# Performance work log

Measured on AMD Instinct MI355X. Metric: run time of the kernel, lower is better.

The kernel has to match this reference:

```python
import jax, jax.numpy as jnp
import numpy as np
import math

Re = 0.15
DX = 1.0
UB = -1.0
NZ, NY, NX = 64, 256, 256
DT = 0.5
ITERATION = 2

def conv3(x, w, stride=1):
    return jax.lax.conv_general_dilated(x, w, (stride, stride, stride), 'VALID', dimension_numbers=('NCDHW', 'OIDHW', 'NCDHW'))

def pad1(x):
    return jnp.pad(x, ((0, 0), (0, 0), (1, 1), (1, 1), (1, 1)))

def bc_u(u):
    p = pad1(u)
    p = p.at[0, 0, :, :, 0].set(UB)
    p = p.at[0, 0, :, :, -1].set(UB)
    p = p.at[0, 0, :, 0, :].set(p[0, 0, :, 1, :])
    p = p.at[0, 0, :, -1, :].set(p[0, 0, :, -2, :])
    p = p.at[0, 0, 0, :, :].set(0.0)
    p = p.at[0, 0, -1, :, :].set(p[0, 0, -2, :, :])
    return p

def bc_v(v):
    # x faces, y faces, z-bottom are zero -> already satisfied by zero padding
    p = pad1(v)
    p = p.at[0, 0, -1, :, :].set(p[0, 0, -2, :, :])
    return p

def bc_w(w):
    # all six faces zero
    return pad1(w)

def bc_p(q):
    p = pad1(q)
    p = p.at[0, 0, :, :, 0].set(p[0, 0, :, :, 1])
    p = p.at[0, 0, :, :, -1].set(0.0)
    p = p.at[0, 0, :, 0, :].set(p[0, 0, :, 1, :])
    p = p.at[0, 0, :, -1, :].set(p[0, 0, :, -2, :])
    p = p.at[0, 0, 0, :, :].set(p[0, 0, 1, :, :])
    p = p.at[0, 0, -1, :, :].set(p[0, 0, -2, :, :])
    return p

def solid_body(u, v, w, sigma, dt):
    s = 1.0 / (1.0 + dt * sigma)
    return u * s, v * s, w * s

def prol(x):
    # nearest-neighbour upsample x2 in z, y, x
    return jnp.repeat(jnp.repeat(jnp.repeat(x, 2, axis=2), 2, axis=3), 2, axis=4)

def all_ads(uu, vv, ww, w1, w2, w3, w4):
    return (conv3(uu, w2), conv3(uu, w3), conv3(uu, w4),
            conv3(vv, w2), conv3(vv, w3), conv3(vv, w4),
            conv3(ww, w2), conv3(ww, w3), conv3(ww, w4),
            conv3(uu, w1), conv3(vv, w1), conv3(ww, w1))

def pg_vector(uu, vv, ww, u, v, w, k1, sigma, dt, w_diff, ads):
    ADx_u, ADy_u, ADz_u, ADx_v, ADy_v, ADz_v, ADx_w, ADy_w, ADz_w, AD2_u, AD2_v, AD2_w = ads
    speed = jnp.abs(u) * DX + jnp.abs(v) * DX + jnp.abs(w) * DX
    c = DX ** -3
    def kd(AD2, ax, ay, az):
        num = 0.1 * DX * jnp.abs((1.0 / 3.0) * c * speed * AD2)
        den = 0.001 + (jnp.abs(ax) * c + jnp.abs(ay) * c + jnp.abs(az) * c) / 3.0
        return num / den
    inv = 1.0 / (1.0 + dt * sigma)
    k_u = jnp.minimum(kd(AD2_u, ADx_u, ADy_u, ADz_u), k1) * inv
    k_v = jnp.minimum(kd(AD2_v, ADx_v, ADy_v, ADz_v), k1) * inv
    k_w = jnp.minimum(kd(AD2_w, ADx_w, ADy_w, ADz_w), k1) * inv
    # boundary_condition_k zeroes every halo face -> plain zero pad
    kuu, kvv, kww = pad1(k_u), pad1(k_v), pad1(k_w)
    k_x = 0.5 * (k_u * AD2_u + conv3(uu * kuu, w_diff) - u * conv3(kuu, w_diff))
    k_y = 0.5 * (k_v * AD2_v + conv3(vv * kvv, w_diff) - v * conv3(kvv, w_diff))
    k_z = 0.5 * (k_w * AD2_w + conv3(ww * kww, w_diff) - w * conv3(kww, w_diff))
    return k_x, k_y, k_z

def f_cycle_mg(uu, vv, ww, p, wA, w2, w3, w4, w_res, iteration, diag, dt, nlevel, ratio_x, ratio_y):
    b = -(conv3(uu, w2) + conv3(vv, w3) + conv3(ww, w4)) / dt
    w = jnp.zeros((1, 1, 2, 2 * ratio_y, 2 * ratio_x), b.dtype)
    r = b
    for _ in range(iteration):
        w = jnp.zeros((1, 1, 2, 2 * ratio_y, 2 * ratio_x), b.dtype)
        r = conv3(bc_p(p), wA) - b
        r_s = [r]
        for _ in range(1, nlevel - 1):
            r = conv3(r, w_res, stride=2)
            r_s.append(r)
        for i in reversed(range(1, nlevel - 1)):
            # boundary_condition_cw zeroes every halo face -> plain zero pad
            w = w - conv3(pad1(w), wA) / diag + r_s[i] / diag
            w = prol(w)
        p = p - w
        p = p - conv3(bc_p(p), wA) / diag + b / diag
    return p, w, r

def forward(values_u, values_v, values_w, values_p, k1, sigma, wA, w1, w2, w3, w4, w_res, dt, iteration):
    nz, ny, nx = values_u.shape[2], values_u.shape[3], values_u.shape[4]
    nlevel = int(math.log2(min(nx, ny, nz))) + 1
    ratio_x, ratio_y = nx // nz, ny // nz
    diag = wA[0, 0, 1, 1, 1]
    u, v, w = solid_body(values_u, values_v, values_w, sigma, dt)
    uu, vv, ww = bc_u(u), bc_v(v), bc_w(w)
    pp = bc_p(values_p)
    Gpx, Gpy, Gpz = conv3(pp, w2) * dt, conv3(pp, w3) * dt, conv3(pp, w4) * dt
    ads = all_ads(uu, vv, ww, w1, w2, w3, w4)
    k_x, k_y, k_z = pg_vector(uu, vv, ww, u, v, w, k1, sigma, dt, w1, ads)
    ADx_u, ADy_u, ADz_u, ADx_v, ADy_v, ADz_v, ADx_w, ADy_w, ADz_w, AD2_u, AD2_v, AD2_w = ads
    # predictor half step
    b_u = u + 0.5 * (Re * AD2_u * dt - u * ADx_u * dt - v * ADy_u * dt - w * ADz_u * dt) + 0.5 * k_x * dt - Gpx
    b_v = v + 0.5 * (Re * AD2_v * dt - u * ADx_v * dt - v * ADy_v * dt - w * ADz_v * dt) + 0.5 * k_y * dt - Gpy
    b_w = w + 0.5 * (Re * AD2_w * dt - u * ADx_w * dt - v * ADy_w * dt - w * ADz_w * dt) + 0.5 * k_z * dt - Gpz
    b_u, b_v, b_w = solid_body(b_u, b_v, b_w, sigma, dt)
    buu, bvv, bww = bc_u(b_u), bc_v(b_v), bc_w(b_w)
    ads = all_ads(buu, bvv, bww, w1, w2, w3, w4)
    k_x, k_y, k_z = pg_vector(buu, bvv, bww, b_u, b_v, b_w, k1, sigma, dt, w1, ads)
    ADx_u, ADy_u, ADz_u, ADx_v, ADy_v, ADz_v, ADx_w, ADy_w, ADz_w, AD2_u, AD2_v, AD2_w = ads
    # corrector full step
    u = u + Re * AD2_u * dt - b_u * ADx_u * dt - b_v * ADy_u * dt - b_w * ADz_u * dt + k_x * dt - Gpx
    v = v + Re * AD2_v * dt - b_u * ADx_v * dt - b_v * ADy_v * dt - b_w * ADz_v * dt + k_y * dt - Gpy
    w = w + Re * AD2_w * dt - b_u * ADx_w * dt - b_v * ADy_w * dt - b_w * ADz_w * dt + k_z * dt - Gpz
    u, v, w = solid_body(u, v, w, sigma, dt)
    uu, vv, ww = bc_u(u), bc_v(v), bc_w(w)
    p, w_mg, r = f_cycle_mg(uu, vv, ww, values_p, wA, w2, w3, w4, w_res, iteration, diag, dt, nlevel, ratio_x, ratio_y)
    # pressure-gradient velocity correction
    pp = bc_p(p)
    u = u - conv3(pp, w2) * dt
    v = v - conv3(pp, w3) * dt
    w = w - conv3(pp, w4) * dt
    u, v, w = solid_body(u, v, w, sigma, dt)
    return u, v, w, p, w_mg, r

def setup_inputs():
    key = jax.random.key(0)
    ks = jax.random.split(key, 4)
    f32 = jnp.float32
    shp = (1, 1, NZ, NY, NX)
    pshp = (1, 1, NZ + 2, NY + 2, NX + 2)
    lap = np.full((3, 3, 3), 1.0 / 26.0, np.float32)
    lap[1, 1, 1] = -1.0
    wA = jnp.asarray(lap.reshape(1, 1, 3, 3, 3))
    w1 = wA / (DX * DX)
    def cdiff(axis):
        k = np.zeros((3, 3, 3), np.float32)
        idx = [1, 1, 1]
        idx[axis] = 0
        k[tuple(idx)] = -0.5
        idx[axis] = 2
        k[tuple(idx)] = 0.5
        return jnp.asarray(k.reshape(1, 1, 3, 3, 3))
    w4, w3, w2 = cdiff(0), cdiff(1), cdiff(2)  # z, y, x advection stencils
    w_res = jnp.full((1, 1, 2, 2, 2), 0.125, f32)
    return dict(
        values_u=0.1 * jax.random.normal(ks[0], shp, f32),
        values_uu=jnp.zeros(pshp, f32),
        values_v=0.1 * jax.random.normal(ks[1], shp, f32),
        values_vv=jnp.zeros(pshp, f32),
        values_w=0.1 * jax.random.normal(ks[2], shp, f32),
        values_ww=jnp.zeros(pshp, f32),
        values_p=0.1 * jax.random.normal(ks[3], shp, f32),
        values_pp=jnp.zeros(pshp, f32),
        b_uu=jnp.zeros(pshp, f32), b_vv=jnp.zeros(pshp, f32), b_ww=jnp.zeros(pshp, f32),
        k1=2.0 * jnp.ones(shp, f32),
        k_uu=jnp.zeros(pshp, f32), k_vv=jnp.zeros(pshp, f32), k_ww=jnp.zeros(pshp, f32),
        sigma=jnp.zeros(shp, f32),
        wA=wA, w1=w1, w2=w2, w3=w3, w4=w4, w_res=w_res,
        dt=DT, iteration=ITERATION,
    )

def reference(values_u, values_uu, values_v, values_vv, values_w, values_ww, values_p, values_pp, b_uu, b_vv, b_ww, k1, k_uu, k_vv, k_ww, sigma, wA, w1, w2, w3, w4, w_res, dt, iteration):
    # padded scratch buffers (values_uu, ..., k_ww) are fully overwritten by the
    # boundary-condition routines, so the functional version rebuilds them via padding
    return forward(values_u, values_v, values_w, values_p, k1, sigma, wA, w1, w2, w3, w4, w_res, dt, iteration)
```

## Files before the change

### kernel.cpp

```cpp
#include <hip/hip_runtime.h>


#define RE_  0.15f
#define UB_  (-1.0f)
#define NZc  64
#define NYc  256
#define NXc  256
#define PZc  (NZc + 2)
#define PYc  (NYc + 2)
#define PXc  (NXc + 2)
#define Ncell  (NZc * NYc * NXc)
#define PNcell (PZc * PYc * PXc)
#define NQ (Ncell / 4)

#define TBX 32
#define TBY 8
#define TZS 16
#define TLX 34
#define TLY 10
#define PL  340

#define NHALO 198920

__device__ __forceinline__ int PIDX(int z, int y, int x) { return (z * PYc + y) * PXc + x; }
__device__ __forceinline__ int IDX (int z, int y, int x) { return (z * NYc + y) * NXc + x; }

struct F1 { float s, c, xm, xp, ym, yp; };
__device__ __forceinline__ F1 rdf1(const float* sl, int ty, int tx) {
  float t[3][3];
#pragma unroll
  for (int dy = 0; dy < 3; ++dy)
#pragma unroll
    for (int dx = 0; dx < 3; ++dx)
      t[dy][dx] = sl[(ty + dy) * TLX + tx + dx];
  F1 f;
  f.s = t[0][0]+t[0][1]+t[0][2]+t[1][0]+t[1][1]+t[1][2]+t[2][0]+t[2][1]+t[2][2];
  f.c = t[1][1]; f.xm = t[1][0]; f.xp = t[1][2]; f.ym = t[0][1]; f.yp = t[2][1];
  return f;
}

struct F2 { float sv, svk, sk, vc, xm, xp, ym, yp, kc; };
__device__ __forceinline__ F2 rdf2(const float* slv, const float* slk, int ty, int tx) {
  float tv[3][3], tk[3][3];
#pragma unroll
  for (int dy = 0; dy < 3; ++dy)
#pragma unroll
    for (int dx = 0; dx < 3; ++dx) {
      tv[dy][dx] = slv[(ty + dy) * TLX + tx + dx];
      tk[dy][dx] = slk[(ty + dy) * TLX + tx + dx];
    }
// ... 25 lines not shown
#define LD3M(T, GA, GB, GC, pz) { \
    int o0 = PIDX((pz), by0 + q0r, bx0 + q0c); \
    (T).a0 = (GA)[o0]; (T).b0 = (GB)[o0]; (T).c0 = (GC)[o0]; \
    if (tid < PL - 256) { int o1 = PIDX((pz), by0 + q1r, bx0 + q1c); \
      (T).a1 = (GA)[o1]; (T).b1 = (GB)[o1]; (T).c1 = (GC)[o1]; } }
#define ST3M(T, slot) { \
    Lu[(slot)][tid] = (T).a0; Lv[(slot)][tid] = (T).b0; Lw[(slot)][tid] = (T).c0; \
    if (tid < PL - 256) { Lu[(slot)][256 + tid] = (T).a1; Lv[(slot)][256 + tid] = (T).b1; \
      Lw[(slot)][256 + tid] = (T).c1; } }
#define LD6M(T, GA, GB, GC, GD, GE, GF, pz) { \
    int o0 = PIDX((pz), by0 + q0r, bx0 + q0c); \
    (T).a0 = (GA)[o0]; (T).b0 = (GB)[o0]; (T).c0 = (GC)[o0]; \
    (T).d0 = (GD)[o0]; (T).e0 = (GE)[o0]; (T).f0 = (GF)[o0]; \
    if (tid < PL - 256) { int o1 = PIDX((pz), by0 + q1r, bx0 + q1c); \
      (T).a1 = (GA)[o1]; (T).b1 = (GB)[o1]; (T).c1 = (GC)[o1]; \
      (T).d1 = (GD)[o1]; (T).e1 = (GE)[o1]; (T).f1 = (GF)[o1]; } }
#define ST6M(T, slot) { \
    Lu[(slot)][tid] = (T).a0; Lv[(slot)][tid] = (T).b0; Lw[(slot)][tid] = (T).c0; \
    Lku[(slot)][tid] = (T).d0; Lkv[(slot)][tid] = (T).e0; Lkw[(slot)][tid] = (T).f0; \
    if (tid < PL - 256) { Lu[(slot)][256 + tid] = (T).a1; Lv[(slot)][256 + tid] = (T).b1; \
      Lw[(slot)][256 + tid] = (T).c1; Lku[(slot)][256 + tid] = (T).d1; \
      Lkv[(slot)][256 + tid] = (T).e1; Lkw[(slot)][256 + tid] = (T).f1; } }

#define TILE_PREAMBLE \
  const int tx = threadIdx.x, ty = threadIdx.y; \
  const int tid = ty * TBX + tx; \
  const int bx0 = blockIdx.x * TBX, by0 = blockIdx.y * TBY; \
  const int z0 = blockIdx.z * TZS; \
  const int q0r = tid / TLX, q0c = tid % TLX; \
  const int q1r = (256 + tid) / TLX, q1c = (256 + tid) % TLX; \
  const int ix = bx0 + tx, iy = by0 + ty;


__global__ __launch_bounds__(256) void k_compute_k_t(
    const float* __restrict__ Au, const float* __restrict__ Av, const float* __restrict__ Aw,
    const float* __restrict__ k1, const float* __restrict__ sigma, const float* __restrict__ dtp,
    const float* __restrict__ w1, const float* __restrict__ wx, const float* __restrict__ wy,
    const float* __restrict__ wz,
    float* __restrict__ Ku, float* __restrict__ Kv, float* __restrict__ Kw) {
  __shared__ float Lu[2][PL], Lv[2][PL], Lw[2][PL];
  TILE_PREAMBLE
  float dt = dtp[0];
  float wo = w1[0], wcd = w1[13] - wo;
  float cxm = wx[12], cxp = wx[14], cym = wy[10], cyp = wy[16], czm = wz[4], czp = wz[22];
  const float third = 1.0f / 3.0f;

  T3 t, tA, tB;
  LD3M(t, Au, Av, Aw, z0); ST3M(t, 0); __syncthreads();
  F1 fu = rdf1(&Lu[0][0], ty, tx), fv = rdf1(&Lv[0][0], ty, tx), fw = rdf1(&Lw[0][0], ty, tx);
  R1s p0u = {fu.s, fu.c}, p0v = {fv.s, fv.c}, p0w = {fw.s, fw.c};
  LD3M(t, Au, Av, Aw, z0 + 1); ST3M(t, 1); __syncthreads();
  F1 p1u = rdf1(&Lu[1][0], ty, tx), p1v = rdf1(&Lv[1][0], ty, tx), p1w = rdf1(&Lw[1][0], ty, tx);
  LD3M(tA, Au, Av, Aw, z0 + 2); ST3M(tA, 0);
  LD3M(tB, Au, Av, Aw, z0 + 3);
  __syncthreads();

  auto body = [&](int iz, int slot) {
    int ci = IDX(iz, iy, ix);
    float inv = 1.0f / (1.0f + dt * sigma[ci]);
    float k1v = k1[ci];
    float speed = fabsf(p1u.c) + fabsf(p1v.c) + fabsf(p1w.c);
    int pc = PIDX(iz + 1, iy + 1, ix + 1);

    fu = rdf1(&Lu[slot][0], ty, tx);
    {
      float ad2 = wo * (p0u.s + p1u.s + fu.s) + wcd * p1u.c;
      float ax = cxm * p1u.xm + cxp * p1u.xp;
      float ay = cym * p1u.ym + cyp * p1u.yp;
      float az = czm * p0u.c + czp * fu.c;
      float num = 0.1f * fabsf(third * speed * ad2);
      float den = 0.001f + (fabsf(ax) + fabsf(ay) + fabsf(az)) * third;
      Ku[pc] = fminf(num / den, k1v) * inv;
    }
    p0u.s = p1u.s; p0u.c = p1u.c; p1u = fu;

    fv = rdf1(&Lv[slot][0], ty, tx);
    {
      float ad2 = wo * (p0v.s + p1v.s + fv.s) + wcd * p1v.c;
      float ax = cxm * p1v.xm + cxp * p1v.xp;
      float ay = cym * p1v.ym + cyp * p1v.yp;
      float az = czm * p0v.c + czp * fv.c;
      float num = 0.1f * fabsf(third * speed * ad2);
      float den = 0.001f + (fabsf(ax) + fabsf(ay) + fabsf(az)) * third;
      Kv[pc] = fminf(num / den, k1v) * inv;
    }
    p0v.s = p1v.s; p0v.c = p1v.c; p1v = fv;

    fw = rdf1(&Lw[slot][0], ty, tx);
    {
      float ad2 = wo * (p0w.s + p1w.s + fw.s) + wcd * p1w.c;
      float ax = cxm * p1w.xm + cxp * p1w.xp;
      float ay = cym * p1w.ym + cyp * p1w.yp;
      float az = czm * p0w.c + czp * fw.c;
      float num = 0.1f * fabsf(third * speed * ad2);
      float den = 0.001f + (fabsf(ax) + fabsf(ay) + fabsf(az)) * third;
      Kw[pc] = fminf(num / den, k1v) * inv;
    }
    p0w.s = p1w.s; p0w.c = p1w.c; p1w = fw;
  };

  for (int iz = z0; iz < z0 + TZS; iz += 2) {
    bool ldA = (iz + 4 <= z0 + TZS + 1);
    if (ldA) LD3M(tA, Au, Av, Aw, iz + 4);
    body(iz, 0);
    ST3M(tB, 1);
    __syncthreads();
    bool ldB = (iz + 5 <= z0 + TZS + 1);
    if (ldB) LD3M(tB, Au, Av, Aw, iz + 5);
    body(iz + 1, 1);
    if (ldA) ST3M(tA, 0);
    __syncthreads();
  }
}

__global__ __launch_bounds__(256) void k_compute_b_t(
    const float* __restrict__ Au, const float* __restrict__ Av, const float* __restrict__ Aw,
    const float* __restrict__ Ku, const float* __restrict__ Kv, const float* __restrict__ Kw,
    const float* __restrict__ gx, const float* __restrict__ gy, const float* __restrict__ gz,
    const float* __restrict__ sigma, const float* __restrict__ dtp,
    const float* __restrict__ w1, const float* __restrict__ wx, const float* __restrict__ wy,
    const float* __restrict__ wz,
    float* __restrict__ Bu, float* __restrict__ Bv, float* __restrict__ Bw) {
  __shared__ float Lu[2][PL], Lv[2][PL], Lw[2][PL], Lku[2][PL], Lkv[2][PL], Lkw[2][PL];
  TILE_PREAMBLE
  float dt = dtp[0];
  float wo = w1[0], wcd = w1[13] - wo;
  float cxm = wx[12], cxp = wx[14], cym = wy[10], cyp = wy[16], czm = wz[4], czp = wz[22];

  T6 t, tA, tB;
  LD6M(t, Au, Av, Aw, Ku, Kv, Kw, z0); ST6M(t, 0); __syncthreads();
  F2 fU = rdf2(&Lu[0][0], &Lku[0][0], ty, tx);
  F2 fV = rdf2(&Lv[0][0], &Lkv[0][0], ty, tx);
  F2 fW = rdf2(&Lw[0][0], &Lkw[0][0], ty, tx);
  R2s p0u = {fU.sv, fU.svk, fU.sk, fU.vc};
  R2s p0v = {fV.sv, fV.svk, fV.sk, fV.vc};
  R2s p0w = {fW.sv, fW.svk, fW.sk, fW.vc};
  LD6M(t, Au, Av, Aw, Ku, Kv, Kw, z0 + 1); ST6M(t, 1); __syncthreads();
  F2 p1u = rdf2(&Lu[1][0], &Lku[1][0], ty, tx);
  F2 p1v = rdf2(&Lv[1][0], &Lkv[1][0], ty, tx);
  F2 p1w = rdf2(&Lw[1][0], &Lkw[1][0], ty, tx);
  LD6M(tA, Au, Av, Aw, Ku, Kv, Kw, z0 + 2); ST6M(tA, 0);
  LD6M(tB, Au, Av, Aw, Ku, Kv, Kw, z0 + 3);
  __syncthreads();

  auto body = [&](int iz, int slot) {
    int ci = IDX(iz, iy, ix);
    float inv = 1.0f / (1.0f + dt * sigma[ci]);
    float gxv = gx[ci], gyv = gy[ci], gzv = gz[ci];
    float uc = p1u.vc, vc = p1v.vc, wc = p1w.vc;
    int pc = PIDX(iz + 1, iy + 1, ix + 1);

    fU = rdf2(&Lu[slot][0], &Lku[slot][0], ty, tx);
    {
      float ad2 = wo * (p0u.sv + p1u.sv + fU.sv) + wcd * uc;
      float suk = wo * (p0u.svk + p1u.svk + fU.svk) + wcd * uc * p1u.kc;
      float sk  = wo * (p0u.sk + p1u.sk + fU.sk) + wcd * p1u.kc;
      float kx = 0.5f * (p1u.kc * ad2 + suk - uc * sk);
      float ax = cxm * p1u.xm + cxp * p1u.xp;
      float ay = cym * p1u.ym + cyp * p1u.yp;
      float az = czm * p0u.vc + czp * fU.vc;
      float bu = uc + 0.5f * dt * (RE_ * ad2 - uc * ax - vc * ay - wc * az) + 0.5f * kx * dt - gxv;
      Bu[pc] = bu * inv;
    }
    p0u.sv = p1u.sv; p0u.svk = p1u.svk; p0u.sk = p1u.sk; p0u.vc = p1u.vc; p1u = fU;

    fV = rdf2(&Lv[slot][0], &Lkv[slot][0], ty, tx);
    {
      float ad2 = wo * (p0v.sv + p1v.sv + fV.sv) + wcd * vc;
      float suk = wo * (p0v.svk + p1v.svk + fV.svk) + wcd * vc * p1v.kc;
      float sk  = wo * (p0v.sk + p1v.sk + fV.sk) + wcd * p1v.kc;
      float kx = 0.5f * (p1v.kc * ad2 + suk - vc * sk);
      float ax = cxm * p1v.xm + cxp * p1v.xp;
      float ay = cym * p1v.ym + cyp * p1v.yp;
      float az = czm * p0v.vc + czp * fV.vc;
      float bv = vc + 0.5f * dt * (RE_ * ad2 - uc * ax - vc * ay - wc * az) + 0.5f * kx * dt - gyv;
      Bv[pc] = bv * inv;
    }
    p0v.sv = p1v.sv; p0v.svk = p1v.svk; p0v.sk = p1v.sk; p0v.vc = p1v.vc; p1v = fV;

    fW = rdf2(&Lw[slot][0], &Lkw[slot][0], ty, tx);
    {
      float ad2 = wo * (p0w.sv + p1w.sv + fW.sv) + wcd * wc;
      float suk = wo * (p0w.svk + p1w.svk + fW.svk) + wcd * wc * p1w.kc;
      float sk  = wo * (p0w.sk + p1w.sk + fW.sk) + wcd * p1w.kc;
      float kx = 0.5f * (p1w.kc * ad2 + suk - wc * sk);
      float ax = cxm * p1w.xm + cxp * p1w.xp;
      float ay = cym * p1w.ym + cyp * p1w.yp;
      float az = czm * p0w.vc + czp * fW.vc;
      float bw = wc + 0.5f * dt * (RE_ * ad2 - uc * ax - vc * ay - wc * az) + 0.5f * kx * dt - gzv;
      Bw[pc] = bw * inv;
    }
    p0w.sv = p1w.sv; p0w.svk = p1w.svk; p0w.sk = p1w.sk; p0w.vc = p1w.vc; p1w = fW;
  };

  for (int iz = z0; iz < z0 + TZS; iz += 2) {
    bool ldA = (iz + 4 <= z0 + TZS + 1);
    if (ldA) LD6M(tA, Au, Av, Aw, Ku, Kv, Kw, iz + 4);
    body(iz, 0);
    ST6M(tB, 1);
    __syncthreads();
    bool ldB = (iz + 5 <= z0 + TZS + 1);
    if (ldB) LD6M(tB, Au, Av, Aw, Ku, Kv, Kw, iz + 5);
    body(iz + 1, 1);
    if (ldA) ST6M(tA, 0);
    __syncthreads();
  }
}

__global__ __launch_bounds__(256) void k_corrector_t(
    float* __restrict__ Au, float* __restrict__ Av, float* __restrict__ Aw,
    const float* __restrict__ Bu, const float* __restrict__ Bv, const float* __restrict__ Bw,
    const float* __restrict__ Ku, const float* __restrict__ Kv, const float* __restrict__ Kw,
    const float* __restrict__ gx, const float* __restrict__ gy, const float* __restrict__ gz,
    const float* __restrict__ sigma, const float* __restrict__ dtp,
    const float* __restrict__ w1, const float* __restrict__ wx, const float* __restrict__ wy,
    const float* __restrict__ wz) {
  __shared__ float Lu[2][PL], Lv[2][PL], Lw[2][PL], Lku[2][PL], Lkv[2][PL], Lkw[2][PL];
  TILE_PREAMBLE
  float dt = dtp[0];
  float wo = w1[0], wcd = w1[13] - wo;
  float cxm = wx[12], cxp = wx[14], cym = wy[10], cyp = wy[16], czm = wz[4], czp = wz[22];

  T6 t, tA, tB;
  LD6M(t, Bu, Bv, Bw, Ku, Kv, Kw, z0); ST6M(t, 0); __syncthreads();
  F2 fU = rdf2(&Lu[0][0], &Lku[0][0], ty, tx);
  F2 fV = rdf2(&Lv[0][0], &Lkv[0][0], ty, tx);
  F2 fW = rdf2(&Lw[0][0], &Lkw[0][0], ty, tx);
  R2s p0u = {fU.sv, fU.svk, fU.sk, fU.vc};
  R2s p0v = {fV.sv, fV.svk, fV.sk, fV.vc};
  R2s p0w = {fW.sv, fW.svk, fW.sk, fW.vc};
  LD6M(t, Bu, Bv, Bw, Ku, Kv, Kw, z0 + 1); ST6M(t, 1); __syncthreads();
  F2 p1u = rdf2(&Lu[1][0], &Lku[1][0], ty, tx);
  F2 p1v = rdf2(&Lv[1][0], &Lkv[1][0], ty, tx);
  F2 p1w = rdf2(&Lw[1][0], &Lkw[1][0], ty, tx);
  LD6M(tA, Bu, Bv, Bw, Ku, Kv, Kw, z0 + 2); ST6M(tA, 0);
  LD6M(tB, Bu, Bv, Bw, Ku, Kv, Kw, z0 + 3);
  __syncthreads();

  auto body = [&](int iz, int slot) {
    int ci = IDX(iz, iy, ix);
    float inv = 1.0f / (1.0f + dt * sigma[ci]);
    float gxv = gx[ci], gyv = gy[ci], gzv = gz[ci];
    int pc = PIDX(iz + 1, iy + 1, ix + 1);
    float auc = Au[pc], avc = Av[pc], awc = Aw[pc];
    float buc = p1u.vc, bvc = p1v.vc, bwc = p1w.vc;

    fU = rdf2(&Lu[slot][0], &Lku[slot][0], ty, tx);
    float un;
    {
      float ad2 = wo * (p0u.sv + p1u.sv + fU.sv) + wcd * buc;
      float suk = wo * (p0u.svk + p1u.svk + fU.svk) + wcd * buc * p1u.kc;
      float sk  = wo * (p0u.sk + p1u.sk + fU.sk) + wcd * p1u.kc;
      float kx = 0.5f * (p1u.kc * ad2 + suk - buc * sk);
      float ax = cxm * p1u.xm + cxp * p1u.xp;
      float ay = cym * p1u.ym + cyp * p1u.yp;
      float az = czm * p0u.vc + czp * fU.vc;
      un = auc + RE_ * ad2 * dt - buc * ax * dt - bvc * ay * dt - bwc * az * dt + kx * dt - gxv;
    }
    p0u.sv = p1u.sv; p0u.svk = p1u.svk; p0u.sk = p1u.sk; p0u.vc = p1u.vc; p1u = fU;

    fV = rdf2(&Lv[slot][0], &Lkv[slot][0], ty, tx);
    float vn;
    {
      float ad2 = wo * (p0v.sv + p1v.sv + fV.sv) + wcd * bvc;
      float suk = wo * (p0v.svk + p1v.svk + fV.svk) + wcd * bvc * p1v.kc;
      float sk  = wo * (p0v.sk + p1v.sk + fV.sk) + wcd * p1v.kc;
      float kx = 0.5f * (p1v.kc * ad2 + suk - bvc * sk);
      float ax = cxm * p1v.xm + cxp * p1v.xp;
      float ay = cym * p1v.ym + cyp * p1v.yp;
      float az = czm * p0v.vc + czp * fV.vc;
      vn = avc + RE_ * ad2 * dt - buc * ax * dt - bvc * ay * dt - bwc * az * dt + kx * dt - gyv;
    }
    p0v.sv = p1v.sv; p0v.svk = p1v.svk; p0v.sk = p1v.sk; p0v.vc = p1v.vc; p1v = fV;

    fW = rdf2(&Lw[slot][0], &Lkw[slot][0], ty, tx);
    float wn;
    {
      float ad2 = wo * (p0w.sv + p1w.sv + fW.sv) + wcd * bwc;
      float suk = wo * (p0w.svk + p1w.svk + fW.svk) + wcd * bwc * p1w.kc;
      float sk  = wo * (p0w.sk + p1w.sk + fW.sk) + wcd * p1w.kc;
      float kx = 0.5f * (p1w.kc * ad2 + suk - bwc * sk);
      float ax = cxm * p1w.xm + cxp * p1w.xp;
      float ay = cym * p1w.ym + cyp * p1w.yp;
      float az = czm * p0w.vc + czp * fW.vc;
      wn = awc + RE_ * ad2 * dt - buc * ax * dt - bvc * ay * dt - bwc * az * dt + kx * dt - gzv;
    }
    p0w.sv = p1w.sv; p0w.svk = p1w.svk; p0w.sk = p1w.sk; p0w.vc = p1w.vc; p1w = fW;

    Au[pc] = un * inv;
    Av[pc] = vn * inv;
    Aw[pc] = wn * inv;
  };

  for (int iz = z0; iz < z0 + TZS; iz += 2) {
    bool ldA = (iz + 4 <= z0 + TZS + 1);
    if (ldA) LD6M(tA, Bu, Bv, Bw, Ku, Kv, Kw, iz + 4);
    body(iz, 0);
    ST6M(tB, 1);
    __syncthreads();
    bool ldB = (iz + 5 <= z0 + TZS + 1);
    if (ldB) LD6M(tB, Bu, Bv, Bw, Ku, Kv, Kw, iz + 5);
    body(iz + 1, 1);
    if (ldA) ST6M(tA, 0);
    __syncthreads();
  }
}

__global__ __launch_bounds__(256) void k_residual_t(
    const float* __restrict__ pp, const float* __restrict__ wA,
    const float* __restrict__ b, float* __restrict__ r0) {
  __shared__ float Lp[2][PL];
  TILE_PREAMBLE
  float wo = wA[0], wcd = wA[13] - wo;

  T1 t, tA, tB;
  LD1M(t, pp, z0); ST1M(t, Lp, 0); __syncthreads();
  F1 f = rdf1(&Lp[0][0], ty, tx);
  R1s p0 = {f.s, f.c};
  LD1M(t, pp, z0 + 1); ST1M(t, Lp, 1); __syncthreads();
  F1 p1 = rdf1(&Lp[1][0], ty, tx);
  LD1M(tA, pp, z0 + 2); ST1M(tA, Lp, 0);
  LD1M(tB, pp, z0 + 3);
  __syncthreads();

  auto body = [&](int iz, int slot) {
    int ci = IDX(iz, iy, ix);
    f = rdf1(&Lp[slot][0], ty, tx);
    r0[ci] = wo * (p0.s + p1.s + f.s) + wcd * p1.c - b[ci];
    p0.s = p1.s; p0.c = p1.c; p1 = f;
  };

  for (int iz = z0; iz < z0 + TZS; iz += 2) {
    bool ldA = (iz + 4 <= z0 + TZS + 1);
    if (ldA) LD1M(tA, pp, iz + 4);
    body(iz, 0);
    ST1M(tB, Lp, 1);
    __syncthreads();
    bool ldB = (iz + 5 <= z0 + TZS + 1);
    if (ldB) LD1M(tB, pp, iz + 5);
    body(iz + 1, 1);
    if (ldA) ST1M(tA, Lp, 0);
    __syncthreads();
  }
}

__global__ __launch_bounds__(256) void k_smooth_t(
    const float* __restrict__ pp, const float* __restrict__ wA,
    const float* __restrict__ b, float* __restrict__ p, float* __restrict__ ppOut) {
  __shared__ float Lp[2][PL];
  TILE_PREAMBLE
  float wo = wA[0], wcd = wA[13] - wo;
  float diag = wA[13];

  T1 t, tA, tB;
  LD1M(t, pp, z0); ST1M(t, Lp, 0); __syncthreads();
  F1 f = rdf1(&Lp[0][0], ty, tx);
  R1s p0 = {f.s, f.c};
  LD1M(t, pp, z0 + 1); ST1M(t, Lp, 1); __syncthreads();
  F1 p1 = rdf1(&Lp[1][0], ty, tx);
  LD1M(tA, pp, z0 + 2); ST1M(tA, Lp, 0);
  LD1M(tB, pp, z0 + 3);
  __syncthreads();

  auto body = [&](int iz, int slot) {
    int ci = IDX(iz, iy, ix);
    f = rdf1(&Lp[slot][0], ty, tx);
    float lap = wo * (p0.s + p1.s + f.s) + wcd * p1.c;
    float v = p1.c - lap / diag + b[ci] / diag;
    p[ci] = v;
    ppOut[PIDX(iz + 1, iy + 1, ix + 1)] = v;
    p0.s = p1.s; p0.c = p1.c; p1 = f;
  };

  for (int iz = z0; iz < z0 + TZS; iz += 2) {
    bool ldA = (iz + 4 <= z0 + TZS + 1);
    if (ldA) LD1M(tA, pp, iz + 4);
    body(iz, 0);
    ST1M(tB, Lp, 1);
    __syncthreads();
    bool ldB = (iz + 5 <= z0 + TZS + 1);
    if (ldB) LD1M(tB, pp, iz + 5);
    body(iz + 1, 1);
    if (ldA) ST1M(tA, Lp, 0);
    __syncthreads();
  }
}


__global__ void k_scale4(const float* __restrict__ u0, const float* __restrict__ v0,
                         const float* __restrict__ w0, const float* __restrict__ sigma,
                         const float* __restrict__ dtp,
                         float* __restrict__ Au, float* __restrict__ Av, float* __restrict__ Aw) {
  int t0 = blockIdx.x * blockDim.x + threadIdx.x;
  if (t0 >= NQ) return;
  float dt = dtp[0];
#pragma unroll
  for (int k = 0; k < 4; ++k) {
    int i = t0 + k * NQ;
    int x = i % NXc; int t = i / NXc; int y = t % NYc; int z = t / NYc;
    float s = 1.0f / (1.0f + dt * sigma[i]);
    int pi = PIDX(z + 1, y + 1, x + 1);
    Au[pi] = u0[i] * s;
    Av[pi] = v0[i] * s;
    Aw[pi] = w0[i] * s;
  }
}

__global__ void k_pad_p4(const float* __restrict__ p, float* __restrict__ pp) {
  int t0 = blockIdx.x * blockDim.x + threadIdx.x;
  if (t0 >= NQ) return;
#pragma unroll
  for (int k = 0; k < 4; ++k) {
    int i = t0 + k * NQ;
    int x = i % NXc; int t = i / NXc; int y = t % NYc; int z = t / NYc;
    pp[PIDX(z + 1, y + 1, x + 1)] = p[i];
  }
}

__global__ void k_grad_p4(const float* __restrict__ pp, const float* __restrict__ wx,
                          const float* __restrict__ wy, const float* __restrict__ wz,
                          const float* __restrict__ dtp,
                          float* __restrict__ gx, float* __restrict__ gy, float* __restrict__ gz) {
  int t0 = blockIdx.x * blockDim.x + threadIdx.x;
  if (t0 >= NQ) return;
  float dt = dtp[0];
  float cxm = wx[12], cxp = wx[14], cym = wy[10], cyp = wy[16], czm = wz[4], czp = wz[22];
#pragma unroll
  for (int k = 0; k < 4; ++k) {
    int i = t0 + k * NQ;
    int x = i % NXc; int t = i / NXc; int y = t % NYc; int z = t / NYc;
    gx[i] = (cxm * pp[PIDX(z + 1, y + 1, x)] + cxp * pp[PIDX(z + 1, y + 1, x + 2)]) * dt;
    gy[i] = (cym * pp[PIDX(z + 1, y, x + 1)] + cyp * pp[PIDX(z + 1, y + 2, x + 1)]) * dt;
    gz[i] = (czm * pp[PIDX(z, y + 1, x + 1)] + czp * pp[PIDX(z + 2, y + 1, x + 1)]) * dt;
  }
}

__global__ void k_divcopy4(const float* __restrict__ Au, const float* __restrict__ Av,
                           const float* __restrict__ Aw, const float* __restrict__ wx,
                           const float* __restrict__ wy, const float* __restrict__ wz,
                           const float* __restrict__ dtp, const float* __restrict__ psrc,
                           float* __restrict__ b, float* __restrict__ pdst) {
  int t0 = blockIdx.x * blockDim.x + threadIdx.x;
  if (t0 >= NQ) return;
  float rdt = 1.0f / dtp[0];
  float cxm = wx[12], cxp = wx[14], cym = wy[10], cyp = wy[16], czm = wz[4], czp = wz[22];
#pragma unroll
  for (int k = 0; k < 4; ++k) {
    int i = t0 + k * NQ;
    int x = i % NXc; int t = i / NXc; int y = t % NYc; int z = t / NYc;
    float dx = cxm * Au[PIDX(z + 1, y + 1, x)] + cxp * Au[PIDX(z + 1, y + 1, x + 2)];
    float dy = cym * Av[PIDX(z + 1, y, x + 1)] + cyp * Av[PIDX(z + 1, y + 2, x + 1)];
    float dz = czm * Aw[PIDX(z, y + 1, x + 1)] + czp * Aw[PIDX(z + 2, y + 1, x + 1)];
    b[i] = -(dx + dy + dz) * rdt;
    pdst[i] = psrc[i];
  }
}

__global__ void k_final4(const float* __restrict__ Au, const float* __restrict__ Av,
                         const float* __restrict__ Aw, const float* __restrict__ pp,
                         const float* __restrict__ wx, const float* __restrict__ wy,
                         const float* __restrict__ wz, const float* __restrict__ sigma,
                         const float* __restrict__ dtp,
                         float* __restrict__ ou, float* __restrict__ ov, float* __restrict__ ow) {
  int t0 = blockIdx.x * blockDim.x + threadIdx.x;
  if (t0 >= NQ) return;
  float dt = dtp[0];
  float cxm = wx[12], cxp = wx[14], cym = wy[10], cyp = wy[16], czm = wz[4], czp = wz[22];
#pragma unroll
  for (int k = 0; k < 4; ++k) {
    int i = t0 + k * NQ;
    int x = i % NXc; int t = i / NXc; int y = t % NYc; int z = t / NYc;
    float inv = 1.0f / (1.0f + dt * sigma[i]);
    int pc = PIDX(z + 1, y + 1, x + 1);
    float dx = cxm * pp[PIDX(z + 1, y + 1, x)] + cxp * pp[PIDX(z + 1, y + 1, x + 2)];
    float dy = cym * pp[PIDX(z + 1, y, x + 1)] + cyp * pp[PIDX(z + 2 + y - y, y + 2, x + 1)];
    dy = cym * pp[PIDX(z + 1, y, x + 1)] + cyp * pp[PIDX(z + 1, y + 2, x + 1)];
    float dz = czm * pp[PIDX(z, y + 1, x + 1)] + czp * pp[PIDX(z + 2, y + 1, x + 1)];
    ou[i] = (Au[pc] - dx * dt) * inv;
    ov[i] = (Av[pc] - dy * dt) * inv;
    ow[i] = (Aw[pc] - dz * dt) * inv;
  }
}

__device__ __forceinline__ void halo_decode(int t, int& z, int& y, int& x) {
  if (t < 2 * PYc * PXc) {
    z = (t >= PYc * PXc) ? PZc - 1 : 0;
    int r = t % (PYc * PXc);
    y = r / PXc; x = r % PXc;
    return;
  }
  t -= 2 * PYc * PXc;
  if (t < 2 * NZc * PXc) {
    z = 1 + t / (2 * PXc);
    int r = t % (2 * PXc);
    y = (r >= PXc) ? PYc - 1 : 0;
    x = r % PXc;
    return;
  }
  t -= 2 * NZc * PXc;
  z = 1 + t / (2 * NYc);
  int r = t % (2 * NYc);
  x = (r >= NYc) ? PXc - 1 : 0;
  y = 1 + (r % NYc);
}

__global__ void k_halo_uvw(float* __restrict__ Au, float* __restrict__ Av, float* __restrict__ Aw) {
  int t = blockIdx.x * blockDim.x + threadIdx.x;
  if (t >= NHALO) return;
  int z, y, x;
// ... 140 lines not shown
extern "C" void kernel_launch(void* const* d_in, const int* in_sizes, int n_in,
                              void* d_out, int out_size, void* d_ws, size_t ws_size,
                              hipStream_t stream) {
  (void)in_sizes; (void)n_in; (void)out_size; (void)ws_size;

  const float* values_u = (const float*)d_in[0];
  const float* values_v = (const float*)d_in[2];
  const float* values_w = (const float*)d_in[4];
  const float* values_p = (const float*)d_in[6];
  const float* k1       = (const float*)d_in[11];
  const float* sigma    = (const float*)d_in[15];
  const float* wA       = (const float*)d_in[16];
  const float* w1       = (const float*)d_in[17];
  const float* w2       = (const float*)d_in[18];
  const float* w3       = (const float*)d_in[19];
  const float* w4       = (const float*)d_in[20];
  const float* wres     = (const float*)d_in[21];
  const float* dtp      = (const float*)d_in[22];
  const int ITER = 2;

  float* ws = (float*)d_ws;
  float* Au = ws + 0ll * PNcell;
  float* Av = ws + 1ll * PNcell;
  float* Aw = ws + 2ll * PNcell;
  float* Ku = ws + 3ll * PNcell;
  float* Kv = ws + 4ll * PNcell;
  float* Kw = ws + 5ll * PNcell;
  float* Bu = ws + 6ll * PNcell;
  float* Bv = ws + 7ll * PNcell;
  float* Bw = ws + 8ll * PNcell;
  float* ppA = ws + 9ll * PNcell;
  float* ppB = Ku;
  float* b_rhs = Bu;
  float* r0    = Bv;
  float* r1  = Bw;
  float* r2  = r1 + 524288;
  float* r3  = r2 + 65536;
  float* r4  = r3 + 8192;
  float* w1b = r4 + 1024;
  float* w2b = w1b + 524288;
  float* w3b = w2b + 65536;
  float* w4b = w3b + 8192;

  float* out_u   = (float*)d_out;
  float* out_v   = out_u + Ncell;
  float* out_w   = out_v + Ncell;
  float* out_p   = out_w + Ncell;
  float* out_wmg = out_p + Ncell;
  float* out_r   = out_wmg + Ncell;
  float* gx = out_u; float* gy = out_v; float* gz = out_w;

  const int B = 256;
  const int gQ = (NQ + B - 1) / B;
  const int gH = (NHALO + B - 1) / B;
  dim3 tblk(TBX, TBY, 1);
  dim3 tgrd(NXc / TBX, NYc / TBY, NZc / TZS);

  k_scale4<<<gQ, B, 0, stream>>>(values_u, values_v, values_w, sigma, dtp, Au, Av, Aw);
  k_halo_uvw<<<gH, B, 0, stream>>>(Au, Av, Aw);
  k_pad_p4<<<gQ, B, 0, stream>>>(values_p, ppA);
  k_halo_p<<<gH, B, 0, stream>>>(ppA);
  k_grad_p4<<<gQ, B, 0, stream>>>(ppA, w2, w3, w4, dtp, gx, gy, gz);

  k_zero_halo3<<<gH, B, 0, stream>>>(Ku, Kv, Kw);
  k_compute_k_t<<<tgrd, tblk, 0, stream>>>(Au, Av, Aw, k1, sigma, dtp, w1, w2, w3, w4, Ku, Kv, Kw);
  k_compute_b_t<<<tgrd, tblk, 0, stream>>>(Au, Av, Aw, Ku, Kv, Kw, gx, gy, gz, sigma, dtp,
                                           w1, w2, w3, w4, Bu, Bv, Bw);
  k_halo_uvw<<<gH, B, 0, stream>>>(Bu, Bv, Bw);

  k_compute_k_t<<<tgrd, tblk, 0, stream>>>(Bu, Bv, Bw, k1, sigma, dtp, w1, w2, w3, w4, Ku, Kv, Kw);
  k_corrector_t<<<tgrd, tblk, 0, stream>>>(Au, Av, Aw, Bu, Bv, Bw, Ku, Kv, Kw, gx, gy, gz,
                                           sigma, dtp, w1, w2, w3, w4);
  k_halo_uvw<<<gH, B, 0, stream>>>(Au, Av, Aw);

  k_divcopy4<<<gQ, B, 0, stream>>>(Au, Av, Aw, w2, w3, w4, dtp, values_p, b_rhs, out_p);
  for (int it = 0; it < ITER; ++it) {
    k_residual_t<<<tgrd, tblk, 0, stream>>>(ppA, wA, b_rhs, r0);
    k_restrict<<<(524288 + B - 1) / B, B, 0, stream>>>(r0, r1, 32, 128, 128, wres);
    k_restrict<<<(65536 + B - 1) / B, B, 0, stream>>>(r1, r2, 16, 64, 64, wres);
    k_restrict<<<(8192 + B - 1) / B, B, 0, stream>>>(r2, r3, 8, 32, 32, wres);
    k_restrict<<<(1024 + B - 1) / B, B, 0, stream>>>(r3, r4, 4, 16, 16, wres);
    k_restrict<<<1, 128, 0, stream>>>(r4, out_r, 2, 8, 8, wres);
    k_up<<<1, 128, 0, stream>>>(nullptr, out_r, w4b, 2, 8, 8, wA, 1);
    k_up<<<(1024 + B - 1) / B, B, 0, stream>>>(w4b, r4, w3b, 4, 16, 16, wA, 0);
    k_up<<<(8192 + B - 1) / B, B, 0, stream>>>(w3b, r3, w2b, 8, 32, 32, wA, 0);
    k_up<<<(65536 + B - 1) / B, B, 0, stream>>>(w2b, r2, w1b, 16, 64, 64, wA, 0);
    k_upsub<<<(524288 + B - 1) / B, B, 0, stream>>>(w1b, r1, wA, out_wmg, out_p, ppB);
    k_halo_p<<<gH, B, 0, stream>>>(ppB);
    k_smooth_t<<<tgrd, tblk, 0, stream>>>(ppB, wA, b_rhs, out_p, ppA);
    k_halo_p<<<gH, B, 0, stream>>>(ppA);
  }

  k_final4<<<gQ, B, 0, stream>>>(Au, Av, Aw, ppA, w2, w3, w4, sigma, dtp, out_u, out_v, out_w);
}
```

Baseline: 792.9 us.

## Fuse residual with first restriction, merge init kernels, shrink z-tiles and simplify pipeline

The residual kernel now does the first 2x2x2 restriction in place, combining z pairs in registers and xy neighbours with lane shuffles, so the full-resolution residual buffer is no longer written and re-read and one launch is dropped. The scale and pressure-pad kernels are merged into one init kernel. All tiled stencil kernels use a shorter z-slab per block and a simpler single-register-stage prefetch loop, with launch bounds raised to ask for more resident blocks per CU. The trade-offs are more halo reloads per slab, less prefetch depth, and reliance on the lane mapping matching the restriction stencil layout.

```diff
diff --git a/kernel.cpp b/kernel.cpp
--- a/kernel.cpp
+++ b/kernel.cpp
@@ -15,7 +15,7 @@
 
 #define TBX 32
 #define TBY 8
-#define TZS 16
+#define TZS 8
 #define TLX 34
 #define TLY 10
 #define PL  340
@@ -107,7 +107,7 @@
   const int ix = bx0 + tx, iy = by0 + ty;
 
 
-__global__ __launch_bounds__(256) void k_compute_k_t(
+__global__ __launch_bounds__(256, 6) void k_compute_k_t(
     const float* __restrict__ Au, const float* __restrict__ Av, const float* __restrict__ Aw,
     const float* __restrict__ k1, const float* __restrict__ sigma, const float* __restrict__ dtp,
     const float* __restrict__ w1, const float* __restrict__ wx, const float* __restrict__ wy,
@@ -120,24 +120,27 @@
   float cxm = wx[12], cxp = wx[14], cym = wy[10], cyp = wy[16], czm = wz[4], czp = wz[22];
   const float third = 1.0f / 3.0f;
 
-  T3 t, tA, tB;
+  T3 t;
   LD3M(t, Au, Av, Aw, z0); ST3M(t, 0); __syncthreads();
   F1 fu = rdf1(&Lu[0][0], ty, tx), fv = rdf1(&Lv[0][0], ty, tx), fw = rdf1(&Lw[0][0], ty, tx);
   R1s p0u = {fu.s, fu.c}, p0v = {fv.s, fv.c}, p0w = {fw.s, fw.c};
   LD3M(t, Au, Av, Aw, z0 + 1); ST3M(t, 1); __syncthreads();
   F1 p1u = rdf1(&Lu[1][0], ty, tx), p1v = rdf1(&Lv[1][0], ty, tx), p1w = rdf1(&Lw[1][0], ty, tx);
-  LD3M(tA, Au, Av, Aw, z0 + 2); ST3M(tA, 0);
-  LD3M(tB, Au, Av, Aw, z0 + 3);
-  __syncthreads();
-
-  auto body = [&](int iz, int slot) {
+  LD3M(t, Au, Av, Aw, z0 + 2); ST3M(t, 0); __syncthreads();
+
+  for (int iz = z0; iz < z0 + TZS; ++iz) {
+    int rs = (iz - z0) & 1, wsl = rs ^ 1;
+    int pzn = iz + 3;
+    bool do_st = (pzn <= z0 + TZS + 1);
+    if (do_st) LD3M(t, Au, Av, Aw, pzn);
+
     int ci = IDX(iz, iy, ix);
     float inv = 1.0f / (1.0f + dt * sigma[ci]);
     float k1v = k1[ci];
     float speed = fabsf(p1u.c) + fabsf(p1v.c) + fabsf(p1w.c);
     int pc = PIDX(iz + 1, iy + 1, ix + 1);
 
-    fu = rdf1(&Lu[slot][0], ty, tx);
+    fu = rdf1(&Lu[rs][0], ty, tx);
     {
       float ad2 = wo * (p0u.s + p1u.s + fu.s) + wcd * p1u.c;
       float ax = cxm * p1u.xm + cxp * p1u.xp;
@@ -149,7 +152,7 @@
     }
     p0u.s = p1u.s; p0u.c = p1u.c; p1u = fu;
 
-    fv = rdf1(&Lv[slot][0], ty, tx);
+    fv = rdf1(&Lv[rs][0], ty, tx);
     {
       float ad2 = wo * (p0v.s + p1v.s + fv.s) + wcd * p1v.c;
       float ax = cxm * p1v.xm + cxp * p1v.xp;
@@ -161,7 +164,7 @@
     }
     p0v.s = p1v.s; p0v.c = p1v.c; p1v = fv;
 
-    fw = rdf1(&Lw[slot][0], ty, tx);
+    fw = rdf1(&Lw[rs][0], ty, tx);
     {
       float ad2 = wo * (p0w.s + p1w.s + fw.s) + wcd * p1w.c;
       float ax = cxm * p1w.xm + cxp * p1w.xp;
@@ -172,23 +175,13 @@
       Kw[pc] = fminf(num / den, k1v) * inv;
     }
     p0w.s = p1w.s; p0w.c = p1w.c; p1w = fw;
-  };
-
-  for (int iz = z0; iz < z0 + TZS; iz += 2) {
-    bool ldA = (iz + 4 <= z0 + TZS + 1);
-    if (ldA) LD3M(tA, Au, Av, Aw, iz + 4);
-    body(iz, 0);
-    ST3M(tB, 1);
+
+    if (do_st) ST3M(t, wsl);
     __syncthreads();
-    bool ldB = (iz + 5 <= z0 + TZS + 1);
-    if (ldB) LD3M(tB, Au, Av, Aw, iz + 5);
-    body(iz + 1, 1);
-    if (ldA) ST3M(tA, 0);
-    __syncthreads();
-  }
-}
-
-__global__ __launch_bounds__(256) void k_compute_b_t(
+  }
+}
+
+__global__ __launch_bounds__(256, 6) void k_compute_b_t(
     const float* __restrict__ Au, const float* __restrict__ Av, const float* __restrict__ Aw,
     const float* __restrict__ Ku, const float* __restrict__ Kv, const float* __restrict__ Kw,
     const float* __restrict__ gx, const float* __restrict__ gy, const float* __restrict__ gz,
@@ -202,7 +195,7 @@
   float wo = w1[0], wcd = w1[13] - wo;
   float cxm = wx[12], cxp = wx[14], cym = wy[10], cyp = wy[16], czm = wz[4], czp = wz[22];
 
-  T6 t, tA, tB;
+  T6 t;
   LD6M(t, Au, Av, Aw, Ku, Kv, Kw, z0); ST6M(t, 0); __syncthreads();
   F2 fU = rdf2(&Lu[0][0], &Lku[0][0], ty, tx);
   F2 fV = rdf2(&Lv[0][0], &Lkv[0][0], ty, tx);
@@ -214,18 +207,21 @@
   F2 p1u = rdf2(&Lu[1][0], &Lku[1][0], ty, tx);
   F2 p1v = rdf2(&Lv[1][0], &Lkv[1][0], ty, tx);
   F2 p1w = rdf2(&Lw[1][0], &Lkw[1][0], ty, tx);
-  LD6M(tA, Au, Av, Aw, Ku, Kv, Kw, z0 + 2); ST6M(tA, 0);
-  LD6M(tB, Au, Av, Aw, Ku, Kv, Kw, z0 + 3);
-  __syncthreads();
-
-  auto body = [&](int iz, int slot) {
+  LD6M(t, Au, Av, Aw, Ku, Kv, Kw, z0 + 2); ST6M(t, 0); __syncthreads();
+
+  for (int iz = z0; iz < z0 + TZS; ++iz) {
+    int rs = (iz - z0) & 1, wsl = rs ^ 1;
+    int pzn = iz + 3;
+    bool do_st = (pzn <= z0 + TZS + 1);
+    if (do_st) LD6M(t, Au, Av, Aw, Ku, Kv, Kw, pzn);
+
     int ci = IDX(iz, iy, ix);
     float inv = 1.0f / (1.0f + dt * sigma[ci]);
     float gxv = gx[ci], gyv = gy[ci], gzv = gz[ci];
     float uc = p1u.vc, vc = p1v.vc, wc = p1w.vc;
     int pc = PIDX(iz + 1, iy + 1, ix + 1);
 
-    fU = rdf2(&Lu[slot][0], &Lku[slot][0], ty, tx);
+    fU = rdf2(&Lu[rs][0], &Lku[rs][0], ty, tx);
     {
       float ad2 = wo * (p0u.sv + p1u.sv + fU.sv) + wcd * uc;
       float suk = wo * (p0u.svk + p1u.svk + fU.svk) + wcd * uc * p1u.kc;
@@ -239,7 +235,7 @@
     }
     p0u.sv = p1u.sv; p0u.svk = p1u.svk; p0u.sk = p1u.sk; p0u.vc = p1u.vc; p1u = fU;
 
-    fV = rdf2(&Lv[slot][0], &Lkv[slot][0], ty, tx);
+    fV = rdf2(&Lv[rs][0], &Lkv[rs][0], ty, tx);
     {
       float ad2 = wo * (p0v.sv + p1v.sv + fV.sv) + wcd * vc;
       float suk = wo * (p0v.svk + p1v.svk + fV.svk) + wcd * vc * p1v.kc;
@@ -253,7 +249,7 @@
     }
     p0v.sv = p1v.sv; p0v.svk = p1v.svk; p0v.sk = p1v.sk; p0v.vc = p1v.vc; p1v = fV;
 
-    fW = rdf2(&Lw[slot][0], &Lkw[slot][0], ty, tx);
+    fW = rdf2(&Lw[rs][0], &Lkw[rs][0], ty, tx);
     {
       float ad2 = wo * (p0w.sv + p1w.sv + fW.sv) + wcd * wc;
       float suk = wo * (p0w.svk + p1w.svk + fW.svk) + wcd * wc * p1w.kc;
@@ -266,23 +262,13 @@
       Bw[pc] = bw * inv;
     }
     p0w.sv = p1w.sv; p0w.svk = p1w.svk; p0w.sk = p1w.sk; p0w.vc = p1w.vc; p1w = fW;
-  };
-
-  for (int iz = z0; iz < z0 + TZS; iz += 2) {
-    bool ldA = (iz + 4 <= z0 + TZS + 1);
-    if (ldA) LD6M(tA, Au, Av, Aw, Ku, Kv, Kw, iz + 4);
-    body(iz, 0);
-    ST6M(tB, 1);
+
+    if (do_st) ST6M(t, wsl);
     __syncthreads();
-    bool ldB = (iz + 5 <= z0 + TZS + 1);
-    if (ldB) LD6M(tB, Au, Av, Aw, Ku, Kv, Kw, iz + 5);
-    body(iz + 1, 1);
-    if (ldA) ST6M(tA, 0);
-    __syncthreads();
-  }
-}
-
-__global__ __launch_bounds__(256) void k_corrector_t(
+  }
+}
+
+__global__ __launch_bounds__(256, 6) void k_corrector_t(
     float* __restrict__ Au, float* __restrict__ Av, float* __restrict__ Aw,
     const float* __restrict__ Bu, const float* __restrict__ Bv, const float* __restrict__ Bw,
     const float* __restrict__ Ku, const float* __restrict__ Kv, const float* __restrict__ Kw,
@@ -296,7 +282,7 @@
   float wo = w1[0], wcd = w1[13] - wo;
   float cxm = wx[12], cxp = wx[14], cym = wy[10], cyp = wy[16], czm = wz[4], czp = wz[22];
 
-  T6 t, tA, tB;
+  T6 t;
   LD6M(t, Bu, Bv, Bw, Ku, Kv, Kw, z0); ST6M(t, 0); __syncthreads();
   F2 fU = rdf2(&Lu[0][0], &Lku[0][0], ty, tx);
   F2 fV = rdf2(&Lv[0][0], &Lkv[0][0], ty, tx);
@@ -308,11 +294,14 @@
   F2 p1u = rdf2(&Lu[1][0], &Lku[1][0], ty, tx);
   F2 p1v = rdf2(&Lv[1][0], &Lkv[1][0], ty, tx);
   F2 p1w = rdf2(&Lw[1][0], &Lkw[1][0], ty, tx);
-  LD6M(tA, Bu, Bv, Bw, Ku, Kv, Kw, z0 + 2); ST6M(tA, 0);
-  LD6M(tB, Bu, Bv, Bw, Ku, Kv, Kw, z0 + 3);
-  __syncthreads();
-
-  auto body = [&](int iz, int slot) {
+  LD6M(t, Bu, Bv, Bw, Ku, Kv, Kw, z0 + 2); ST6M(t, 0); __syncthreads();
+
+  for (int iz = z0; iz < z0 + TZS; ++iz) {
+    int rs = (iz - z0) & 1, wsl = rs ^ 1;
+    int pzn = iz + 3;
+    bool do_st = (pzn <= z0 + TZS + 1);
+    if (do_st) LD6M(t, Bu, Bv, Bw, Ku, Kv, Kw, pzn);
+
     int ci = IDX(iz, iy, ix);
     float inv = 1.0f / (1.0f + dt * sigma[ci]);
     float gxv = gx[ci], gyv = gy[ci], gzv = gz[ci];
@@ -320,7 +309,7 @@
     float auc = Au[pc], avc = Av[pc], awc = Aw[pc];
     float buc = p1u.vc, bvc = p1v.vc, bwc = p1w.vc;
 
-    fU = rdf2(&Lu[slot][0], &Lku[slot][0], ty, tx);
+    fU = rdf2(&Lu[rs][0], &Lku[rs][0], ty, tx);
     float un;
     {
       float ad2 = wo * (p0u.sv + p1u.sv + fU.sv) + wcd * buc;
@@ -334,7 +323,7 @@
     }
     p0u.sv = p1u.sv; p0u.svk = p1u.svk; p0u.sk = p1u.sk; p0u.vc = p1u.vc; p1u = fU;
 
-    fV = rdf2(&Lv[slot][0], &Lkv[slot][0], ty, tx);
+    fV = rdf2(&Lv[rs][0], &Lkv[rs][0], ty, tx);
     float vn;
     {
       float ad2 = wo * (p0v.sv + p1v.sv + fV.sv) + wcd * bvc;
@@ -348,7 +337,7 @@
     }
     p0v.sv = p1v.sv; p0v.svk = p1v.svk; p0v.sk = p1v.sk; p0v.vc = p1v.vc; p1v = fV;
 
-    fW = rdf2(&Lw[slot][0], &Lkw[slot][0], ty, tx);
+    fW = rdf2(&Lw[rs][0], &Lkw[rs][0], ty, tx);
     float wn;
     {
       float ad2 = wo * (p0w.sv + p1w.sv + fW.sv) + wcd * bwc;
@@ -365,61 +354,55 @@
     Au[pc] = un * inv;
     Av[pc] = vn * inv;
     Aw[pc] = wn * inv;
-  };
-
-  for (int iz = z0; iz < z0 + TZS; iz += 2) {
-    bool ldA = (iz + 4 <= z0 + TZS + 1);
-    if (ldA) LD6M(tA, Bu, Bv, Bw, Ku, Kv, Kw, iz + 4);
-    body(iz, 0);
-    ST6M(tB, 1);
+
+    if (do_st) ST6M(t, wsl);
     __syncthreads();
-    bool ldB = (iz + 5 <= z0 + TZS + 1);
-    if (ldB) LD6M(tB, Bu, Bv, Bw, Ku, Kv, Kw, iz + 5);
-    body(iz + 1, 1);
-    if (ldA) ST6M(tA, 0);
-    __syncthreads();
-  }
-}
-
-__global__ __launch_bounds__(256) void k_residual_t(
+  }
+}
+
+__global__ __launch_bounds__(256, 6) void k_residual_t(
     const float* __restrict__ pp, const float* __restrict__ wA,
-    const float* __restrict__ b, float* __restrict__ r0) {
+    const float* __restrict__ b, float* __restrict__ r1,
+    const float* __restrict__ wres) {
   __shared__ float Lp[2][PL];
   TILE_PREAMBLE
   float wo = wA[0], wcd = wA[13] - wo;
-
-  T1 t, tA, tB;
+  float w_ev = wres[((ty & 1) << 1) | (tx & 1)];
+  float w_od = wres[4 + (((ty & 1) << 1) | (tx & 1))];
+
+  T1 t;
   LD1M(t, pp, z0); ST1M(t, Lp, 0); __syncthreads();
   F1 f = rdf1(&Lp[0][0], ty, tx);
   R1s p0 = {f.s, f.c};
   LD1M(t, pp, z0 + 1); ST1M(t, Lp, 1); __syncthreads();
   F1 p1 = rdf1(&Lp[1][0], ty, tx);
-  LD1M(tA, pp, z0 + 2); ST1M(tA, Lp, 0);
-  LD1M(tB, pp, z0 + 3);
-  __syncthreads();
-
-  auto body = [&](int iz, int slot) {
+  LD1M(t, pp, z0 + 2); ST1M(t, Lp, 0); __syncthreads();
+
+  float r_ev = 0.f;
+  for (int iz = z0; iz < z0 + TZS; ++iz) {
+    int rs = (iz - z0) & 1, wsl = rs ^ 1;
+    int pzn = iz + 3;
+    bool do_st = (pzn <= z0 + TZS + 1);
+    if (do_st) LD1M(t, pp, pzn);
     int ci = IDX(iz, iy, ix);
-    f = rdf1(&Lp[slot][0], ty, tx);
-    r0[ci] = wo * (p0.s + p1.s + f.s) + wcd * p1.c - b[ci];
+    f = rdf1(&Lp[rs][0], ty, tx);
+    float rv = wo * (p0.s + p1.s + f.s) + wcd * p1.c - b[ci];
     p0.s = p1.s; p0.c = p1.c; p1 = f;
-  };
-
-  for (int iz = z0; iz < z0 + TZS; iz += 2) {
-    bool ldA = (iz + 4 <= z0 + TZS + 1);
-    if (ldA) LD1M(tA, pp, iz + 4);
-    body(iz, 0);
-    ST1M(tB, Lp, 1);
+    if ((iz & 1) == 0) {
+      r_ev = rv;
+    } else {
+      float c = w_ev * r_ev + w_od * rv;
+      c += __shfl_xor(c, 1);
+      c += __shfl_xor(c, 32);
+      if (((tx | ty) & 1) == 0)
+        r1[((iz >> 1) * 128 + (iy >> 1)) * 128 + (ix >> 1)] = c;
+    }
+    if (do_st) ST1M(t, Lp, wsl);
     __syncthreads();
-    bool ldB = (iz + 5 <= z0 + TZS + 1);
-    if (ldB) LD1M(tB, pp, iz + 5);
-    body(iz + 1, 1);
-    if (ldA) ST1M(tA, Lp, 0);
-    __syncthreads();
-  }
-}
-
-__global__ __launch_bounds__(256) void k_smooth_t(
+  }
+}
+
+__global__ __launch_bounds__(256, 6) void k_smooth_t(
     const float* __restrict__ pp, const float* __restrict__ wA,
     const float* __restrict__ b, float* __restrict__ p, float* __restrict__ ppOut) {
   __shared__ float Lp[2][PL];
@@ -427,45 +410,37 @@
   float wo = wA[0], wcd = wA[13] - wo;
   float diag = wA[13];
 
-  T1 t, tA, tB;
+  T1 t;
   LD1M(t, pp, z0); ST1M(t, Lp, 0); __syncthreads();
   F1 f = rdf1(&Lp[0][0], ty, tx);
   R1s p0 = {f.s, f.c};
   LD1M(t, pp, z0 + 1); ST1M(t, Lp, 1); __syncthreads();
   F1 p1 = rdf1(&Lp[1][0], ty, tx);
-  LD1M(tA, pp, z0 + 2); ST1M(tA, Lp, 0);
-  LD1M(tB, pp, z0 + 3);
-  __syncthreads();
-
-  auto body = [&](int iz, int slot) {
+  LD1M(t, pp, z0 + 2); ST1M(t, Lp, 0); __syncthreads();
+
+  for (int iz = z0; iz < z0 + TZS; ++iz) {
+    int rs = (iz - z0) & 1, wsl = rs ^ 1;
+    int pzn = iz + 3;
+    bool do_st = (pzn <= z0 + TZS + 1);
+    if (do_st) LD1M(t, pp, pzn);
     int ci = IDX(iz, iy, ix);
-    f = rdf1(&Lp[slot][0], ty, tx);
+    f = rdf1(&Lp[rs][0], ty, tx);
     float lap = wo * (p0.s + p1.s + f.s) + wcd * p1.c;
     float v = p1.c - lap / diag + b[ci] / diag;
     p[ci] = v;
     ppOut[PIDX(iz + 1, iy + 1, ix + 1)] = v;
     p0.s = p1.s; p0.c = p1.c; p1 = f;
-  };
-
-  for (int iz = z0; iz < z0 + TZS; iz += 2) {
-    bool ldA = (iz + 4 <= z0 + TZS + 1);
-    if (ldA) LD1M(tA, pp, iz + 4);
-    body(iz, 0);
-    ST1M(tB, Lp, 1);
+    if (do_st) ST1M(t, Lp, wsl);
     __syncthreads();
-    bool ldB = (iz + 5 <= z0 + TZS + 1);
-    if (ldB) LD1M(tB, pp, iz + 5);
-    body(iz + 1, 1);
-    if (ldA) ST1M(tA, Lp, 0);
-    __syncthreads();
-  }
-}
-
-
-__global__ void k_scale4(const float* __restrict__ u0, const float* __restrict__ v0,
-                         const float* __restrict__ w0, const float* __restrict__ sigma,
-                         const float* __restrict__ dtp,
-                         float* __restrict__ Au, float* __restrict__ Av, float* __restrict__ Aw) {
+  }
+}
+
+
+__global__ void k_init4(const float* __restrict__ u0, const float* __restrict__ v0,
+                        const float* __restrict__ w0, const float* __restrict__ sigma,
+                        const float* __restrict__ p, const float* __restrict__ dtp,
+                        float* __restrict__ Au, float* __restrict__ Av, float* __restrict__ Aw,
+                        float* __restrict__ pp) {
   int t0 = blockIdx.x * blockDim.x + threadIdx.x;
   if (t0 >= NQ) return;
   float dt = dtp[0];
@@ -478,17 +453,7 @@
     Au[pi] = u0[i] * s;
     Av[pi] = v0[i] * s;
     Aw[pi] = w0[i] * s;
-  }
-}
-
-__global__ void k_pad_p4(const float* __restrict__ p, float* __restrict__ pp) {
-  int t0 = blockIdx.x * blockDim.x + threadIdx.x;
-  if (t0 >= NQ) return;
-#pragma unroll
-  for (int k = 0; k < 4; ++k) {
-    int i = t0 + k * NQ;
-    int x = i % NXc; int t = i / NXc; int y = t % NYc; int z = t / NYc;
-    pp[PIDX(z + 1, y + 1, x + 1)] = p[i];
+    pp[pi] = p[i];
   }
 }
 
@@ -548,8 +513,7 @@
     float inv = 1.0f / (1.0f + dt * sigma[i]);
     int pc = PIDX(z + 1, y + 1, x + 1);
     float dx = cxm * pp[PIDX(z + 1, y + 1, x)] + cxp * pp[PIDX(z + 1, y + 1, x + 2)];
-    float dy = cym * pp[PIDX(z + 1, y, x + 1)] + cyp * pp[PIDX(z + 2 + y - y, y + 2, x + 1)];
-    dy = cym * pp[PIDX(z + 1, y, x + 1)] + cyp * pp[PIDX(z + 1, y + 2, x + 1)];
+    float dy = cym * pp[PIDX(z + 1, y, x + 1)] + cyp * pp[PIDX(z + 1, y + 2, x + 1)];
     float dz = czm * pp[PIDX(z, y + 1, x + 1)] + czp * pp[PIDX(z + 2, y + 1, x + 1)];
     ou[i] = (Au[pc] - dx * dt) * inv;
     ov[i] = (Av[pc] - dy * dt) * inv;
@@ -756,7 +720,6 @@
   float* ppA = ws + 9ll * PNcell;
   float* ppB = Ku;
   float* b_rhs = Bu;
-  float* r0    = Bv;
   float* r1  = Bw;
   float* r2  = r1 + 524288;
   float* r3  = r2 + 65536;
@@ -780,9 +743,9 @@
   dim3 tblk(TBX, TBY, 1);
   dim3 tgrd(NXc / TBX, NYc / TBY, NZc / TZS);
 
-  k_scale4<<<gQ, B, 0, stream>>>(values_u, values_v, values_w, sigma, dtp, Au, Av, Aw);
+  k_init4<<<gQ, B, 0, stream>>>(values_u, values_v, values_w, sigma, values_p, dtp,
+                                Au, Av, Aw, ppA);
   k_halo_uvw<<<gH, B, 0, stream>>>(Au, Av, Aw);
-  k_pad_p4<<<gQ, B, 0, stream>>>(values_p, ppA);
   k_halo_p<<<gH, B, 0, stream>>>(ppA);
   k_grad_p4<<<gQ, B, 0, stream>>>(ppA, w2, w3, w4, dtp, gx, gy, gz);
 
@@ -799,8 +762,7 @@
 
   k_divcopy4<<<gQ, B, 0, stream>>>(Au, Av, Aw, w2, w3, w4, dtp, values_p, b_rhs, out_p);
   for (int it = 0; it < ITER; ++it) {
-    k_residual_t<<<tgrd, tblk, 0, stream>>>(ppA, wA, b_rhs, r0);
-    k_restrict<<<(524288 + B - 1) / B, B, 0, stream>>>(r0, r1, 32, 128, 128, wres);
+    k_residual_t<<<tgrd, tblk, 0, stream>>>(ppA, wA, b_rhs, r1, wres);
     k_restrict<<<(65536 + B - 1) / B, B, 0, stream>>>(r1, r2, 16, 64, 64, wres);
     k_restrict<<<(8192 + B - 1) / B, B, 0, stream>>>(r2, r3, 8, 32, 32, wres);
     k_restrict<<<(1024 + B - 1) / B, B, 0, stream>>>(r3, r4, 4, 16, 16, wres);
```

Result: slower. 1.474 ms (+85.9%).
